# Performance work log

Measured on AMD Instinct MI355X. Metric: run time of the kernel, lower is better.

## Reference

```python
import jax, jax.numpy as jnp
import numpy as np

BN_EPS = 1e-5
K_HOPS = 10


def setup_inputs() -> dict:
    key = jax.random.key(0)
    ks = jax.random.split(key, 8)
    N, F, H, C, E = 169343, 128, 256, 40, 1200000
    return {
        "x": jax.random.normal(ks[0], (N, F), dtype=jnp.float32),
        "edge_index": jax.random.randint(ks[1], (2, E), 0, N, dtype=jnp.int64),
        "norm": jax.random.uniform(ks[2], (E,), dtype=jnp.float32),
        "W1": jax.random.normal(ks[3], (F, H), dtype=jnp.float32) * (1.0 / np.sqrt(F)),
        "b1": jnp.zeros((H,), jnp.float32),
        "bn_gamma": jnp.ones((H,), jnp.float32),
        "bn_beta": jnp.zeros((H,), jnp.float32),
        "bn_mean": jnp.zeros((H,), jnp.float32),
        "bn_var": jnp.ones((H,), jnp.float32),
        "W2": jax.random.normal(ks[4], (H, C), dtype=jnp.float32) * (1.0 / np.sqrt(H)),
        "b2": jnp.zeros((C,), jnp.float32),
        "proj_w": jax.random.normal(ks[5], (C,), dtype=jnp.float32) * (1.0 / np.sqrt(C)),
        "proj_b": jnp.zeros((1,), jnp.float32),
    }


def reference(x, edge_index, norm, W1, b1, bn_gamma, bn_beta, bn_mean, bn_var,
              W2, b2, proj_w, proj_b):
    N = x.shape[0]
    src, dst = edge_index[0], edge_index[1]

    # MLP head: Linear -> BatchNorm (eval, running stats) -> ReLU -> Linear
    h = x @ W1 + b1
    h = (h - bn_mean) * jax.lax.rsqrt(bn_var + BN_EPS) * bn_gamma + bn_beta
    h = jax.nn.relu(h)  # dropout: identity at inference
    h = h @ W2 + b2  # [N, C]

    # K-hop norm-weighted scatter-add propagation, collecting snapshots
    def hop(carry, _):
        msgs = norm[:, None] * carry[src]              # [E, C]
        nxt = jax.ops.segment_sum(msgs, dst, num_segments=N)
        return nxt, nxt

    _, hops = jax.lax.scan(hop, h, None, length=K_HOPS)  # [K, N, C]
    pps = jnp.concatenate([h[None], hops], axis=0)       # [K+1, N, C]
    pps = jnp.transpose(pps, (1, 0, 2))                  # [N, K+1, C]

    # sigmoid attention over hops, weighted combine
    retain = jax.nn.sigmoid(pps @ proj_w + proj_b[0])    # [N, K+1]
    out = jnp.einsum("nk,nkc->nc", retain, pps)          # [N, C]
    return jax.nn.log_softmax(out, axis=1)
```

## Files before the change

### kernel.cpp

```cpp
#include <hip/hip_runtime.h>
#include <hip/hip_bf16.h>
#include <math.h>

#define F 128
#define H 256
#define C 40
#define KHOPS 10
#define TM 32

typedef short bf16x8 __attribute__((ext_vector_type(8)));
typedef float f32x4 __attribute__((ext_vector_type(4)));

__device__ __forceinline__ void split3(float v, ushort& s1, ushort& s2, ushort& s3) {
    unsigned u = __float_as_uint(v);
    float f1 = __uint_as_float(u & 0xFFFF0000u);
    s1 = (ushort)(u >> 16);
    float r = v - f1;
    unsigned ur = __float_as_uint(r);
    float f2 = __uint_as_float(ur & 0xFFFF0000u);
    s2 = (ushort)(ur >> 16);
    float r2 = r - f2;
    s3 = (ushort)(__float_as_uint(r2) >> 16);
}

__global__ void k_count(const int* __restrict__ dst, int E, int* __restrict__ cnt) {
    int e = blockIdx.x * 256 + threadIdx.x;
    if (e < E) atomicAdd(&cnt[dst[e]], 1);
}

__global__ void k_scan1(const int* __restrict__ cnt, int n, int* __restrict__ bsum) {
    __shared__ int sh[256];
    int t = threadIdx.x;
    int base = blockIdx.x * 4096 + t * 16;
    int s = 0;
    for (int i = 0; i < 16; i++) { int idx = base + i; if (idx < n) s += cnt[idx]; }
    sh[t] = s; __syncthreads();
    for (int o = 128; o > 0; o >>= 1) {
        if (t < o) sh[t] += sh[t + o];
        __syncthreads();
    }
    if (t == 0) bsum[blockIdx.x] = sh[0];
}

__global__ void k_scan2(int* __restrict__ bsum, int nb) {
    if (threadIdx.x == 0) {
        int acc = 0;
        for (int i = 0; i < nb; i++) { int v = bsum[i]; bsum[i] = acc; acc += v; }
    }
}

__global__ void k_scan3(const int* __restrict__ cnt, int n, const int* __restrict__ bsum,
                        int* __restrict__ rp) {
    __shared__ int sh[256];
    int t = threadIdx.x;
    int base = blockIdx.x * 4096 + t * 16;
    int local[16]; int s = 0;
    for (int i = 0; i < 16; i++) {
        int idx = base + i;
        int v = (idx < n) ? cnt[idx] : 0;
        local[i] = v; s += v;
    }
    sh[t] = s; __syncthreads();
    for (int o = 1; o < 256; o <<= 1) {
        int v = (t >= o) ? sh[t - o] : 0;
        __syncthreads();
        sh[t] += v;
        __syncthreads();
    }
    int excl = (t == 0) ? 0 : sh[t - 1];
    int run = bsum[blockIdx.x] + excl;
    for (int i = 0; i < 16; i++) {
        int idx = base + i;
        if (idx < n) { rp[idx] = run; run += local[i]; }
    }
}

__global__ void k_fill(const int* __restrict__ src, const int* __restrict__ dst,
                       const float* __restrict__ nrm, int E, const int* __restrict__ rp,
                       int* __restrict__ cur, int2* __restrict__ ep) {
    int e = blockIdx.x * 256 + threadIdx.x;
    if (e < E) {
        int d = dst[e];
        int p = rp[d] + atomicAdd(&cur[d], 1);
        ep[p] = make_int2(src[e], __float_as_int(nrm[e]));
    }
}

__global__ void k_wsplit(const float* __restrict__ W1, ushort* __restrict__ w1a,
                         ushort* __restrict__ w1b, ushort* __restrict__ w1c) {
    int t = blockIdx.x * 256 + threadIdx.x;
    if (t < F * H) {
        int h = t / F, f = t % F;
        ushort a, b, c;
        split3(W1[(size_t)f * H + h], a, b, c);
        w1a[t] = a; w1b[t] = b; w1c[t] = c;
    }
}

__launch_bounds__(256, 3)
__global__ void k_mlp(const float* __restrict__ x,
                      const ushort* __restrict__ w1a, const ushort* __restrict__ w1b,
                      const ushort* __restrict__ w1c,
                      const float* __restrict__ b1, const float* __restrict__ g,
                      const float* __restrict__ be, const float* __restrict__ mu,
                      const float* __restrict__ var, const float* __restrict__ W2,
                      const float* __restrict__ b2, const float* __restrict__ pw,
                      const float* __restrict__ pb,
                      float* __restrict__ hbuf, float* __restrict__ oacc, int N) {
    __shared__ float xs[TM][132];
    __shared__ float h1s[TM][260];
    __shared__ float ascS[H], dscS[H];
    __shared__ float sigv[TM];

    int t = threadIdx.x;
    int n0 = blockIdx.x * TM;

    for (int kk = 0; kk < 4; kk++) {
        int idx = kk * 256 + t;
        int node = idx >> 5, f4 = idx & 31;
        int n = n0 + node;
        float4 v = (n < N) ? ((const float4*)x)[(size_t)n * (F / 4) + f4]
                           : make_float4(0.f, 0.f, 0.f, 0.f);
        *((float4*)&xs[node][f4 * 4]) = v;
    }
    {
        float a = g[t] * rsqrtf(var[t] + 1e-5f);
        ascS[t] = a;
        dscS[t] = (b1[t] - mu[t]) * a + be[t];
    }
    __syncthreads();

    int lane = t & 63, wv = t >> 6, quad = lane >> 4, lq = lane & 15;
    int n0w = wv * 64;
    f32x4 acc[2][4];
    #pragma unroll
    for (int mi = 0; mi < 2; mi++)
        #pragma unroll
        for (int ni = 0; ni < 4; ni++)
            acc[mi][ni] = (f32x4){0.f, 0.f, 0.f, 0.f};

    #pragma unroll
    for (int ks = 0; ks < 4; ks++) {
        int k0 = ks * 32 + quad * 8;
        bf16x8 a1[2], a2[2], a3[2];
        #pragma unroll
        for (int mi = 0; mi < 2; mi++) {
            int row = mi * 16 + lq;
            float4 f0 = *((const float4*)&xs[row][k0]);
            float4 f1 = *((const float4*)&xs[row][k0 + 4]);
            float fv[8] = {f0.x, f0.y, f0.z, f0.w, f1.x, f1.y, f1.z, f1.w};
            #pragma unroll
            for (int e = 0; e < 8; e++) {
                ushort sa, sb, sc;
                split3(fv[e], sa, sb, sc);
                a1[mi][e] = (short)sa; a2[mi][e] = (short)sb; a3[mi][e] = (short)sc;
            }
        }
        #pragma unroll
        for (int ni = 0; ni < 4; ni++) {
            size_t wo = (size_t)(n0w + ni * 16 + lq) * F + k0;
            bf16x8 q1 = *((const bf16x8*)(w1a + wo));
            bf16x8 q2 = *((const bf16x8*)(w1b + wo));
            bf16x8 q3 = *((const bf16x8*)(w1c + wo));
            #pragma unroll
            for (int mi = 0; mi < 2; mi++) {
                acc[mi][ni] = __builtin_amdgcn_mfma_f32_16x16x32_bf16(a1[mi], q1, acc[mi][ni], 0, 0, 0);
                acc[mi][ni] = __builtin_amdgcn_mfma_f32_16x16x32_bf16(a1[mi], q2, acc[mi][ni], 0, 0, 0);
                acc[mi][ni] = __builtin_amdgcn_mfma_f32_16x16x32_bf16(a2[mi], q1, acc[mi][ni], 0, 0, 0);
                acc[mi][ni] = __builtin_amdgcn_mfma_f32_16x16x32_bf16(a1[mi], q3, acc[mi][ni], 0, 0, 0);
                acc[mi][ni] = __builtin_amdgcn_mfma_f32_16x16x32_bf16(a2[mi], q2, acc[mi][ni], 0, 0, 0);
                acc[mi][ni] = __builtin_amdgcn_mfma_f32_16x16x32_bf16(a3[mi], q1, acc[mi][ni], 0, 0, 0);
            }
        }
    }

    #pragma unroll
    for (int ni = 0; ni < 4; ni++) {
        int h = n0w + ni * 16 + lq;
        float a = ascS[h], d = dscS[h];
        #pragma unroll
        for (int mi = 0; mi < 2; mi++) {
            #pragma unroll
            for (int r = 0; r < 4; r++) {
                int node = mi * 16 + quad * 4 + r;
                float v = acc[mi][ni][r] * a + d;
                h1s[node][h] = v > 0.f ? v : 0.f;
            }
        }
    }
    __syncthreads();

    int kh = t >> 7;
    int u  = t & 127;
    int ng = u >> 3;
    int cg = u & 7;
    float acc2[2][5];
    #pragma unroll
    for (int j = 0; j < 5; j++) { acc2[0][j] = 0.f; acc2[1][j] = 0.f; }

    float (*w2s)[68] = (float (*)[68])&xs[0][0];

    for (int ch = 0; ch < 4; ch++) {
        for (int kk = 0; kk < 10; kk++) {
            int idx = kk * 256 + t;
            if (idx < 2560) {
                int hh = idx / 40, c = idx % 40;
                w2s[c][hh] = W2[(size_t)(ch * 64 + hh) * C + c];
            }
        }
        __syncthreads();
        if ((ch >> 1) == kh) {
            int hb = ch * 64;
            #pragma unroll 2
            for (int hh = 0; hh < 64; hh += 4) {
                float4 ha = *((const float4*)&h1s[ng][hb + hh]);
                float4 hc = *((const float4*)&h1s[ng + 16][hb + hh]);
                #pragma unroll
                for (int j = 0; j < 5; j++) {
                    float4 w4 = *((const float4*)&w2s[cg * 5 + j][hh]);
                    acc2[0][j] += ha.x * w4.x + ha.y * w4.y + ha.z * w4.z + ha.w * w4.w;
                    acc2[1][j] += hc.x * w4.x + hc.y * w4.y + hc.z * w4.z + hc.w * w4.w;
                }
            }
        }
        __syncthreads();
    }

    float (*pbuf)[40] = (float (*)[40])&xs[0][0];
    if (kh == 1) {
        #pragma unroll
        for (int j = 0; j < 5; j++) {
            pbuf[ng][cg * 5 + j] = acc2[0][j];
            pbuf[ng + 16][cg * 5 + j] = acc2[1][j];
        }
    }
    __syncthreads();
    if (kh == 0) {
        float p0 = 0.f, p1 = 0.f;
        #pragma unroll
        for (int j = 0; j < 5; j++) {
            int c = cg * 5 + j;
            float bb = b2[c];
            float h0 = acc2[0][j] + pbuf[ng][c] + bb;
            float h1v = acc2[1][j] + pbuf[ng + 16][c] + bb;
            float wv2 = pw[c];
            p0 += h0 * wv2;
            p1 += h1v * wv2;
            h1s[ng][c] = h0;
            h1s[ng + 16][c] = h1v;
        }
        #pragma unroll
        for (int m = 1; m < 8; m <<= 1) {
            p0 += __shfl_xor(p0, m);
            p1 += __shfl_xor(p1, m);
        }
        if (cg == 0) {
            sigv[ng]      = 1.f / (1.f + expf(-(p0 + pb[0])));
            sigv[ng + 16] = 1.f / (1.f + expf(-(p1 + pb[0])));
        }
    }
    __syncthreads();

    if (t < 160) {
        int row = t / 5, p = t % 5;
        int n = n0 + row;
        if (n < N) {
            float4 a, b;
            a.x = h1s[row][8 * p + 0]; a.y = h1s[row][8 * p + 1];
            a.z = h1s[row][8 * p + 2]; a.w = h1s[row][8 * p + 3];
            b.x = h1s[row][8 * p + 4]; b.y = h1s[row][8 * p + 5];
            b.z = h1s[row][8 * p + 6]; b.w = h1s[row][8 * p + 7];
            float4* hp = (float4*)(hbuf + (size_t)n * C + 8 * p);
            hp[0] = a; hp[1] = b;
            float sg = sigv[row];
            float4 oa, ob;
            oa.x = sg * a.x; oa.y = sg * a.y; oa.z = sg * a.z; oa.w = sg * a.w;
            ob.x = sg * b.x; ob.y = sg * b.y; ob.z = sg * b.z; ob.w = sg * b.w;
            float4* op = (float4*)(oacc + (size_t)n * C + 8 * p);
            op[0] = oa; op[1] = ob;
        }
    }
}

__global__ void k_hop(const float4* __restrict__ cur4, float4* __restrict__ nxt4,
                      float4* __restrict__ oacc4, const int* __restrict__ rp,
                      const int2* __restrict__ ep,
                      const float* __restrict__ pw, const float* __restrict__ pb,
                      int N, int last) {
    __shared__ float red[320];
    __shared__ float sig[64];
    __shared__ float statm[64];
    __shared__ float stats[64];
    int t = threadIdx.x;
    int nl = t / 5, p = t % 5;
    int n = blockIdx.x * 64 + nl;
    int c0 = 2 * p;
    float4 a0 = make_float4(0.f, 0.f, 0.f, 0.f);
    float4 a1 = make_float4(0.f, 0.f, 0.f, 0.f);
    if (n < N) {
        int b = rp[n], e = rp[n + 1];
        int j = b;
        for (; j + 4 <= e; j += 4) {
            int2 e0 = ep[j], e1 = ep[j + 1], e2 = ep[j + 2], e3 = ep[j + 3];
            const float4* r0 = cur4 + (size_t)e0.x * 10 + c0;
            const float4* r1 = cur4 + (size_t)e1.x * 10 + c0;
            const float4* r2 = cur4 + (size_t)e2.x * 10 + c0;
            const float4* r3 = cur4 + (size_t)e3.x * 10 + c0;
            float4 v00 = r0[0], v01 = r0[1];
            float4 v10 = r1[0], v11 = r1[1];
            float4 v20 = r2[0], v21 = r2[1];
            float4 v30 = r3[0], v31 = r3[1];
            float w0 = __int_as_float(e0.y), w1 = __int_as_float(e1.y);
            float w2 = __int_as_float(e2.y), w3 = __int_as_float(e3.y);
            a0.x += w0 * v00.x; a0.y += w0 * v00.y; a0.z += w0 * v00.z; a0.w += w0 * v00.w;
            a1.x += w0 * v01.x; a1.y += w0 * v01.y; a1.z += w0 * v01.z; a1.w += w0 * v01.w;
            a0.x += w1 * v10.x; a0.y += w1 * v10.y; a0.z += w1 * v10.z; a0.w += w1 * v10.w;
            a1.x += w1 * v11.x; a1.y += w1 * v11.y; a1.z += w1 * v11.z; a1.w += w1 * v11.w;
            a0.x += w2 * v20.x; a0.y += w2 * v20.y; a0.z += w2 * v20.z; a0.w += w2 * v20.w;
            a1.x += w2 * v21.x; a1.y += w2 * v21.y; a1.z += w2 * v21.z; a1.w += w2 * v21.w;
            a0.x += w3 * v30.x; a0.y += w3 * v30.y; a0.z += w3 * v30.z; a0.w += w3 * v30.w;
            a1.x += w3 * v31.x; a1.y += w3 * v31.y; a1.z += w3 * v31.z; a1.w += w3 * v31.w;
        }
        if (j + 2 <= e) {
            int2 e0 = ep[j], e1 = ep[j + 1];
            const float4* r0 = cur4 + (size_t)e0.x * 10 + c0;
            const float4* r1 = cur4 + (size_t)e1.x * 10 + c0;
            float4 v00 = r0[0], v01 = r0[1];
            float4 v10 = r1[0], v11 = r1[1];
            float w0 = __int_as_float(e0.y), w1 = __int_as_float(e1.y);
            a0.x += w0 * v00.x; a0.y += w0 * v00.y; a0.z += w0 * v00.z; a0.w += w0 * v00.w;
            a1.x += w0 * v01.x; a1.y += w0 * v01.y; a1.z += w0 * v01.z; a1.w += w0 * v01.w;
            a0.x += w1 * v10.x; a0.y += w1 * v10.y; a0.z += w1 * v10.z; a0.w += w1 * v10.w;
            a1.x += w1 * v11.x; a1.y += w1 * v11.y; a1.z += w1 * v11.z; a1.w += w1 * v11.w;
            j += 2;
        }
        if (j < e) {
            int2 e0 = ep[j];
            const float4* r0 = cur4 + (size_t)e0.x * 10 + c0;
            float4 v00 = r0[0], v01 = r0[1];
            float w0 = __int_as_float(e0.y);
            a0.x += w0 * v00.x; a0.y += w0 * v00.y; a0.z += w0 * v00.z; a0.w += w0 * v00.w;
            a1.x += w0 * v01.x; a1.y += w0 * v01.y; a1.z += w0 * v01.z; a1.w += w0 * v01.w;
        }
        if (!last) {
            nxt4[(size_t)n * 10 + c0] = a0;
            nxt4[(size_t)n * 10 + c0 + 1] = a1;
        }
    }
    float4 pw0 = ((const float4*)pw)[c0];
    float4 pw1 = ((const float4*)pw)[c0 + 1];
    red[t] = a0.x * pw0.x + a0.y * pw0.y + a0.z * pw0.z + a0.w * pw0.w
           + a1.x * pw1.x + a1.y * pw1.y + a1.z * pw1.z + a1.w * pw1.w;
    __syncthreads();
    if (p == 0) {
        float s = red[t] + red[t + 1] + red[t + 2] + red[t + 3] + red[t + 4];
        sig[nl] = 1.f / (1.f + expf(-(s + pb[0])));
    }
    __syncthreads();
    float4 v0 = make_float4(0.f, 0.f, 0.f, 0.f);
    float4 v1 = make_float4(0.f, 0.f, 0.f, 0.f);
    size_t o = (size_t)n * 10 + c0;
    if (n < N) {
        float sg = sig[nl];
        v0 = oacc4[o]; v1 = oacc4[o + 1];
        v0.x += sg * a0.x; v0.y += sg * a0.y; v0.z += sg * a0.z; v0.w += sg * a0.w;
        v1.x += sg * a1.x; v1.y += sg * a1.y; v1.z += sg * a1.z; v1.w += sg * a1.w;
        if (!last) {
            oacc4[o] = v0;
            oacc4[o + 1] = v1;
        }
    }
    if (last) {
        bool ok = n < N;
        float mx = fmaxf(fmaxf(fmaxf(v0.x, v0.y), fmaxf(v0.z, v0.w)),
                         fmaxf(fmaxf(v1.x, v1.y), fmaxf(v1.z, v1.w)));
        red[t] = ok ? mx : -1e30f;
        __syncthreads();
        if (p == 0) {
            float m = fmaxf(fmaxf(fmaxf(red[t], red[t + 1]), fmaxf(red[t + 2], red[t + 3])),
                            red[t + 4]);
            statm[nl] = m;
        }
        __syncthreads();
        float m = statm[nl];
        float s = 0.f;
        if (ok) {
            s = expf(v0.x - m) + expf(v0.y - m) + expf(v0.z - m) + expf(v0.w - m)
              + expf(v1.x - m) + expf(v1.y - m) + expf(v1.z - m) + expf(v1.w - m);
        }
        red[t] = s;
        __syncthreads();
        if (p == 0) {
            float ssum = red[t] + red[t + 1] + red[t + 2] + red[t + 3] + red[t + 4];
            stats[nl] = logf(ssum);
        }
        __syncthreads();
        if (ok) {
            float ls = statm[nl] + stats[nl];
            oacc4[o]     = make_float4(v0.x - ls, v0.y - ls, v0.z - ls, v0.w - ls);
            oacc4[o + 1] = make_float4(v1.x - ls, v1.y - ls, v1.z - ls, v1.w - ls);
        }
    }
}

extern "C" void kernel_launch(void* const* d_in, const int* in_sizes, int n_in,
                              void* d_out, int out_size, void* d_ws, size_t ws_size,
                              hipStream_t stream) {
    const float* x   = (const float*)d_in[0];
    const int*   ei  = (const int*)d_in[1];
    const float* nrm = (const float*)d_in[2];
    const float* W1  = (const float*)d_in[3];
    const float* b1  = (const float*)d_in[4];
    const float* g   = (const float*)d_in[5];
    const float* be  = (const float*)d_in[6];
    const float* mu  = (const float*)d_in[7];
    const float* var = (const float*)d_in[8];
    const float* W2  = (const float*)d_in[9];
    const float* b2  = (const float*)d_in[10];
    const float* pw  = (const float*)d_in[11];
    const float* pb  = (const float*)d_in[12];
    float* out = (float*)d_out;

    int N = in_sizes[0] / F;
    int E = in_sizes[2];

    char* w = (char*)d_ws;
    auto alloc = [&](size_t bytes) {
        void* p = (void*)w;
        w += ((bytes + 255) / 256) * 256;
        return p;
    };
    int*    rp     = (int*)alloc((size_t)(N + 1) * 4);
    int*    cursor = (int*)alloc((size_t)(N + 1) * 4);
    int*    bsum   = (int*)alloc(1024);
    int2*   ep     = (int2*)alloc((size_t)E * 8);
    ushort* w1a    = (ushort*)alloc((size_t)F * H * 2);
    ushort* w1b    = (ushort*)alloc((size_t)F * H * 2);
    ushort* w1c    = (ushort*)alloc((size_t)F * H * 2);
    float*  bufA   = (float*)alloc((size_t)N * C * 4);
    float*  bufB   = (float*)alloc((size_t)N * C * 4);

    hipMemsetAsync(cursor, 0, (size_t)(N + 1) * 4, stream);

    k_count<<<(E + 255) / 256, 256, 0, stream>>>(ei + E, E, cursor);

    int n1 = N + 1;
    int NB = (n1 + 4095) / 4096;
    k_scan1<<<NB, 256, 0, stream>>>(cursor, n1, bsum);
    k_scan2<<<1, 64, 0, stream>>>(bsum, NB);
    k_scan3<<<NB, 256, 0, stream>>>(cursor, n1, bsum, rp);

    hipMemsetAsync(cursor, 0, (size_t)(N + 1) * 4, stream);
    k_fill<<<(E + 255) / 256, 256, 0, stream>>>(ei, ei + E, nrm, E, rp, cursor, ep);

    k_wsplit<<<(F * H + 255) / 256, 256, 0, stream>>>(W1, w1a, w1b, w1c);

    k_mlp<<<(N + TM - 1) / TM, 256, 0, stream>>>(x, w1a, w1b, w1c, b1, g, be, mu, var,
                                                 W2, b2, pw, pb, bufA, out, N);

    int nodeBlocks64 = (N + 63) / 64;
    float* cur = bufA;
    float* nxt = bufB;
    for (int k = 0; k < KHOPS; k++) {
        k_hop<<<nodeBlocks64, 320, 0, stream>>>((const float4*)cur, (float4*)nxt, (float4*)out,
                                                rp, ep, pw, pb, N, (k == KHOPS - 1) ? 1 : 0);
        float* tmp = cur; cur = nxt; nxt = tmp;
    }
}
```

Baseline: 1.045 ms.

## Run second MLP layer on MFMA with split-bf16 emulated FP32

Replaces the scalar FP32 FMA loop for the H->C second linear layer with bf16 MFMA instructions, using a three-way bf16 split of both operands (six products) to keep near-FP32 accuracy. W2 is pre-split and padded to 48 columns by a new small kernel, and each wave computes a 64-wide K slice whose partials are reduced through shared memory. This removes the per-block W2 staging loop and its syncs and moves the arithmetic to matrix cores. In exchange it adds on-the-fly splitting of activations, padded work, and a four-way shared-memory reduction.

```diff
diff --git a/kernel.cpp b/kernel.cpp
--- a/kernel.cpp
+++ b/kernel.cpp
@@ -5,6 +5,7 @@
 #define F 128
 #define H 256
 #define C 40
+#define CP 48
 #define KHOPS 10
 #define TM 32
 
@@ -97,13 +98,27 @@
     }
 }
 
+__global__ void k_w2split(const float* __restrict__ W2, ushort* __restrict__ w2a,
+                          ushort* __restrict__ w2b, ushort* __restrict__ w2c) {
+    int t = blockIdx.x * 256 + threadIdx.x;
+    if (t < CP * H) {
+        int c = t / H, k = t % H;
+        float v = (c < C) ? W2[(size_t)k * C + c] : 0.f;
+        ushort a, b, cc;
+        split3(v, a, b, cc);
+        w2a[t] = a; w2b[t] = b; w2c[t] = cc;
+    }
+}
+
 __launch_bounds__(256, 3)
 __global__ void k_mlp(const float* __restrict__ x,
                       const ushort* __restrict__ w1a, const ushort* __restrict__ w1b,
                       const ushort* __restrict__ w1c,
+                      const ushort* __restrict__ w2a, const ushort* __restrict__ w2b,
+                      const ushort* __restrict__ w2c,
                       const float* __restrict__ b1, const float* __restrict__ g,
                       const float* __restrict__ be, const float* __restrict__ mu,
-                      const float* __restrict__ var, const float* __restrict__ W2,
+                      const float* __restrict__ var,
                       const float* __restrict__ b2, const float* __restrict__ pw,
                       const float* __restrict__ pb,
                       float* __restrict__ hbuf, float* __restrict__ oacc, int N) {
@@ -190,74 +205,80 @@
     }
     __syncthreads();
 
-    int kh = t >> 7;
-    int u  = t & 127;
-    int ng = u >> 3;
-    int cg = u & 7;
-    float acc2[2][5];
-    #pragma unroll
-    for (int j = 0; j < 5; j++) { acc2[0][j] = 0.f; acc2[1][j] = 0.f; }
-
-    float (*w2s)[68] = (float (*)[68])&xs[0][0];
-
-    for (int ch = 0; ch < 4; ch++) {
-        for (int kk = 0; kk < 10; kk++) {
-            int idx = kk * 256 + t;
-            if (idx < 2560) {
-                int hh = idx / 40, c = idx % 40;
-                w2s[c][hh] = W2[(size_t)(ch * 64 + hh) * C + c];
-            }
-        }
-        __syncthreads();
-        if ((ch >> 1) == kh) {
-            int hb = ch * 64;
-            #pragma unroll 2
-            for (int hh = 0; hh < 64; hh += 4) {
-                float4 ha = *((const float4*)&h1s[ng][hb + hh]);
-                float4 hc = *((const float4*)&h1s[ng + 16][hb + hh]);
-                #pragma unroll
-                for (int j = 0; j < 5; j++) {
-                    float4 w4 = *((const float4*)&w2s[cg * 5 + j][hh]);
-                    acc2[0][j] += ha.x * w4.x + ha.y * w4.y + ha.z * w4.z + ha.w * w4.w;
-                    acc2[1][j] += hc.x * w4.x + hc.y * w4.y + hc.z * w4.z + hc.w * w4.w;
-                }
-            }
-        }
-        __syncthreads();
-    }
-
-    float (*pbuf)[40] = (float (*)[40])&xs[0][0];
-    if (kh == 1) {
-        #pragma unroll
-        for (int j = 0; j < 5; j++) {
-            pbuf[ng][cg * 5 + j] = acc2[0][j];
-            pbuf[ng + 16][cg * 5 + j] = acc2[1][j];
-        }
-    }
-    __syncthreads();
-    if (kh == 0) {
-        float p0 = 0.f, p1 = 0.f;
+    f32x4 acc2[2][3];
+    #pragma unroll
+    for (int mi = 0; mi < 2; mi++)
+        #pragma unroll
+        for (int ni = 0; ni < 3; ni++)
+            acc2[mi][ni] = (f32x4){0.f, 0.f, 0.f, 0.f};
+
+    int kb0 = wv * 64;
+    #pragma unroll
+    for (int ks2 = 0; ks2 < 2; ks2++) {
+        int k0 = kb0 + ks2 * 32 + quad * 8;
+        bf16x8 a1[2], a2[2], a3[2];
+        #pragma unroll
+        for (int mi = 0; mi < 2; mi++) {
+            int row = mi * 16 + lq;
+            float4 f0 = *((const float4*)&h1s[row][k0]);
+            float4 f1 = *((const float4*)&h1s[row][k0 + 4]);
+            float fv[8] = {f0.x, f0.y, f0.z, f0.w, f1.x, f1.y, f1.z, f1.w};
+            #pragma unroll
+            for (int e = 0; e < 8; e++) {
+                ushort sa, sb, sc;
+                split3(fv[e], sa, sb, sc);
+                a1[mi][e] = (short)sa; a2[mi][e] = (short)sb; a3[mi][e] = (short)sc;
+            }
+        }
+        #pragma unroll
+        for (int ni = 0; ni < 3; ni++) {
+            size_t wo = (size_t)(ni * 16 + lq) * H + k0;
+            bf16x8 q1 = *((const bf16x8*)(w2a + wo));
+            bf16x8 q2 = *((const bf16x8*)(w2b + wo));
+            bf16x8 q3 = *((const bf16x8*)(w2c + wo));
+            #pragma unroll
+            for (int mi = 0; mi < 2; mi++) {
+                acc2[mi][ni] = __builtin_amdgcn_mfma_f32_16x16x32_bf16(a1[mi], q1, acc2[mi][ni], 0, 0, 0);
+                acc2[mi][ni] = __builtin_amdgcn_mfma_f32_16x16x32_bf16(a1[mi], q2, acc2[mi][ni], 0, 0, 0);
+                acc2[mi][ni] = __builtin_amdgcn_mfma_f32_16x16x32_bf16(a2[mi], q1, acc2[mi][ni], 0, 0, 0);
+                acc2[mi][ni] = __builtin_amdgcn_mfma_f32_16x16x32_bf16(a1[mi], q3, acc2[mi][ni], 0, 0, 0);
+                acc2[mi][ni] = __builtin_amdgcn_mfma_f32_16x16x32_bf16(a2[mi], q2, acc2[mi][ni], 0, 0, 0);
+                acc2[mi][ni] = __builtin_amdgcn_mfma_f32_16x16x32_bf16(a3[mi], q1, acc2[mi][ni], 0, 0, 0);
+            }
+        }
+    }
+    __syncthreads();
+
+    float* pbB = &h1s[0][0];
+    #pragma unroll
+    for (int mi = 0; mi < 2; mi++)
+        #pragma unroll
+        for (int ni = 0; ni < 3; ni++)
+            #pragma unroll
+            for (int r = 0; r < 4; r++) {
+                int node = mi * 16 + quad * 4 + r;
+                int c = ni * 16 + lq;
+                pbB[wv * (TM * CP) + node * CP + c] = acc2[mi][ni][r];
+            }
+    __syncthreads();
+
+    float* hrow = &h1s[0][0] + 4 * TM * CP;
+    {
+        int ng = t >> 3, cg = t & 7;
+        float p = 0.f;
         #pragma unroll
         for (int j = 0; j < 5; j++) {
             int c = cg * 5 + j;
-            float bb = b2[c];
-            float h0 = acc2[0][j] + pbuf[ng][c] + bb;
-            float h1v = acc2[1][j] + pbuf[ng + 16][c] + bb;
-            float wv2 = pw[c];
-            p0 += h0 * wv2;
-            p1 += h1v * wv2;
-            h1s[ng][c] = h0;
-            h1s[ng + 16][c] = h1v;
-        }
-        #pragma unroll
-        for (int m = 1; m < 8; m <<= 1) {
-            p0 += __shfl_xor(p0, m);
-            p1 += __shfl_xor(p1, m);
-        }
-        if (cg == 0) {
-            sigv[ng]      = 1.f / (1.f + expf(-(p0 + pb[0])));
-            sigv[ng + 16] = 1.f / (1.f + expf(-(p1 + pb[0])));
-        }
+            float h = pbB[0 * (TM * CP) + ng * CP + c]
+                    + pbB[1 * (TM * CP) + ng * CP + c]
+                    + pbB[2 * (TM * CP) + ng * CP + c]
+                    + pbB[3 * (TM * CP) + ng * CP + c] + b2[c];
+            hrow[ng * C + c] = h;
+            p += h * pw[c];
+        }
+        #pragma unroll
+        for (int m = 1; m < 8; m <<= 1) p += __shfl_xor(p, m);
+        if (cg == 0) sigv[ng] = 1.f / (1.f + expf(-(p + pb[0])));
     }
     __syncthreads();
 
@@ -265,11 +286,8 @@
         int row = t / 5, p = t % 5;
         int n = n0 + row;
         if (n < N) {
-            float4 a, b;
-            a.x = h1s[row][8 * p + 0]; a.y = h1s[row][8 * p + 1];
-            a.z = h1s[row][8 * p + 2]; a.w = h1s[row][8 * p + 3];
-            b.x = h1s[row][8 * p + 4]; b.y = h1s[row][8 * p + 5];
-            b.z = h1s[row][8 * p + 6]; b.w = h1s[row][8 * p + 7];
+            float4 a = *((const float4*)&hrow[row * C + 8 * p]);
+            float4 b = *((const float4*)&hrow[row * C + 8 * p + 4]);
             float4* hp = (float4*)(hbuf + (size_t)n * C + 8 * p);
             hp[0] = a; hp[1] = b;
             float sg = sigv[row];
@@ -437,6 +455,9 @@
     ushort* w1a    = (ushort*)alloc((size_t)F * H * 2);
     ushort* w1b    = (ushort*)alloc((size_t)F * H * 2);
     ushort* w1c    = (ushort*)alloc((size_t)F * H * 2);
+    ushort* w2a    = (ushort*)alloc((size_t)CP * H * 2);
+    ushort* w2b    = (ushort*)alloc((size_t)CP * H * 2);
+    ushort* w2c    = (ushort*)alloc((size_t)CP * H * 2);
     float*  bufA   = (float*)alloc((size_t)N * C * 4);
     float*  bufB   = (float*)alloc((size_t)N * C * 4);
 
@@ -454,9 +475,11 @@
     k_fill<<<(E + 255) / 256, 256, 0, stream>>>(ei, ei + E, nrm, E, rp, cursor, ep);
 
     k_wsplit<<<(F * H + 255) / 256, 256, 0, stream>>>(W1, w1a, w1b, w1c);
-
-    k_mlp<<<(N + TM - 1) / TM, 256, 0, stream>>>(x, w1a, w1b, w1c, b1, g, be, mu, var,
-                                                 W2, b2, pw, pb, bufA, out, N);
+    k_w2split<<<(CP * H + 255) / 256, 256, 0, stream>>>(W2, w2a, w2b, w2c);
+
+    k_mlp<<<(N + TM - 1) / TM, 256, 0, stream>>>(x, w1a, w1b, w1c, w2a, w2b, w2c,
+                                                 b1, g, be, mu, var,
+                                                 b2, pw, pb, bufA, out, N);
 
     int nodeBlocks64 = (N + 63) / 64;
     float* cur = bufA;
```

After: 1.004 ms. -4.0%, faster.
